# Kernel tuning notes

Hardware: AMD Instinct MI355X
Metric: run time of the kernel (lower is better)

The kernel has to match this reference:

```python
import jax, jax.numpy as jnp
import numpy as np

HIDDEN = 1024
HEADS = 16
HEAD_DIM = HIDDEN // HEADS  # 64


def setup_inputs() -> dict:
    key = jax.random.key(0)
    kx, kqkv, ko = jax.random.split(key, 3)
    x = jax.random.normal(kx, (2, 2048, HIDDEN), dtype=jnp.float32)
    # Xavier-uniform init like the torch module; torch Linear weight is [out, in]
    lim_qkv = float(np.sqrt(6.0 / (HIDDEN + 3 * HIDDEN)))
    qkv_w = jax.random.uniform(kqkv, (3 * HIDDEN, HIDDEN), minval=-lim_qkv, maxval=lim_qkv, dtype=jnp.float32)
    qkv_b = jnp.zeros((3 * HIDDEN,), dtype=jnp.float32)
    lim_o = float(np.sqrt(6.0 / (HIDDEN + HIDDEN)))
    o_w = jax.random.uniform(ko, (HIDDEN, HIDDEN), minval=-lim_o, maxval=lim_o, dtype=jnp.float32)
    o_b = jnp.zeros((HIDDEN,), dtype=jnp.float32)
    return {"x": x, "qkv_w": qkv_w, "qkv_b": qkv_b, "o_w": o_w, "o_b": o_b}


def reference(x, qkv_w, qkv_b, o_w, o_b):
    B, S, D = x.shape
    H, Dh = HEADS, HEAD_DIM
    # qkv projection (torch Linear: x @ W.T + b) -> [B, S, 3*D]
    qkv = jnp.einsum('bsd,ed->bse', x, qkv_w) + qkv_b
    # reshape to [B, H, S, 3*Dh] then split into q, k, v
    qkv = qkv.reshape(B, S, H, 3 * Dh).transpose(0, 2, 1, 3)
    q, k, v = jnp.split(qkv, 3, axis=-1)  # each [B, H, S, Dh]
    # scaled dot-product attention, materializing full [B, H, S, S] scores
    logits = jnp.einsum('bhqd,bhkd->bhqk', q, k) / jnp.sqrt(jnp.asarray(Dh, x.dtype))
    attn = jax.nn.softmax(logits, axis=-1)
    values = jnp.einsum('bhqk,bhkd->bhqd', attn, v)
    # merge heads -> [B, S, D], then output projection
    values = values.transpose(0, 2, 1, 3).reshape(B, S, D)
    return jnp.einsum('bsd,ed->bse', values, o_w) + o_b
```

## Files before the change

kernel.cpp:

```cpp
#include <hip/hip_runtime.h>
#include <hip/hip_bf16.h>

#define BDIM 2
#define SEQ  2048
#define HID  1024
#define NH   16
#define HD   64
#define MROWS (BDIM * SEQ)
#define QKVN  (3 * HID)
#define QBLK 128

typedef __attribute__((ext_vector_type(8))) short s8b;
typedef __attribute__((ext_vector_type(4))) float f4;

__device__ __forceinline__ unsigned f2bf(float f) {
    unsigned u = __builtin_bit_cast(unsigned, f);
    return (u + 0x7FFFu + ((u >> 16) & 1u)) >> 16;
}
__device__ __forceinline__ float bf2f(unsigned h) {
    return __builtin_bit_cast(float, h << 16);
}

__global__ __launch_bounds__(256) void split_hi_lo(
    const float* __restrict__ src, unsigned short* __restrict__ hi,
    unsigned short* __restrict__ lo, int n8)
{
    const int i = blockIdx.x * 256 + threadIdx.x;
    if (i >= n8) return;
    const float4* s = (const float4*)src + 2 * (size_t)i;
    float4 a = s[0], b = s[1];
    const float v[8] = {a.x, a.y, a.z, a.w, b.x, b.y, b.z, b.w};
    unsigned hu[8], lu[8];
#pragma unroll
    for (int j = 0; j < 8; ++j) {
        hu[j] = f2bf(v[j]);
        lu[j] = f2bf(v[j] - bf2f(hu[j]));
    }
    uint4 hv = {hu[0] | (hu[1] << 16), hu[2] | (hu[3] << 16),
                hu[4] | (hu[5] << 16), hu[6] | (hu[7] << 16)};
    uint4 lv = {lu[0] | (lu[1] << 16), lu[2] | (lu[3] << 16),
                lu[4] | (lu[5] << 16), lu[6] | (lu[7] << 16)};
    *((uint4*)hi + i) = hv;
    *((uint4*)lo + i) = lv;
}

template <int OUTBF>
__global__ __launch_bounds__(256)
__attribute__((amdgpu_waves_per_eu(2, 2)))
void gemm_split(
    const unsigned short* __restrict__ Ah, const unsigned short* __restrict__ Al,
    const unsigned short* __restrict__ Wh, const unsigned short* __restrict__ Wl,
    const float* __restrict__ bias, void* __restrict__ Cout, int N, int K)
{
    const int t   = threadIdx.x;
    const int l   = t & 63;
    const int l15 = t & 15;
    const int lg  = (t >> 4) & 3;
    const int w   = t >> 6;
    const int wr  = w >> 1, wc = w & 1;
    const int bm  = blockIdx.y * 128, bn = blockIdx.x * 128;

    __shared__ unsigned short SB[2][4][128 * 32];

    f4 acc[4][4];
#pragma unroll
    for (int i = 0; i < 4; ++i)
#pragma unroll
        for (int j = 0; j < 4; ++j) acc[i][j] = (f4){0.f, 0.f, 0.f, 0.f};

    const unsigned short* plane_src = (w == 0) ? Ah : (w == 1) ? Al
                                    : (w == 2) ? Wh : Wl;
    const int rb0 = (w < 2) ? bm : bn;
    const int gsw = ((l & 3) ^ ((l >> 2) & 3)) * 8;

    auto stage = [&](int buf, int k0) {
        const unsigned short* gp =
            plane_src + (size_t)(rb0 + (l >> 2)) * K + k0 + gsw;
        unsigned short* lb = &SB[buf][w][0];
#pragma unroll
        for (int c = 0; c < 8; ++c)
            __builtin_amdgcn_global_load_lds(
                (const __attribute__((address_space(1))) void*)(gp + (size_t)(c * 16) * K),
                (__attribute__((address_space(3))) void*)(lb + c * 512),
                16, 0, 0);
    };

    const int ksw = ((lg ^ (l15 & 3)) & 3) << 3;

    stage(0, 0);
    __syncthreads();

    int cur = 0;
    const int nsteps = K >> 5;
    for (int step = 0; step < nsteps; ++step) {
        if (step + 1 < nsteps) stage(cur ^ 1, (step + 1) << 5);

        const unsigned short* base = &SB[cur][0][0];
        s8b bh[4], bl[4];
#pragma unroll
        for (int nt = 0; nt < 4; ++nt) {
            const int ro = (wc * 64 + nt * 16 + l15) * 32 + ksw;
            bh[nt] = *(const s8b*)(base + 2 * 4096 + ro);
            bl[nt] = *(const s8b*)(base + 3 * 4096 + ro);
        }
#pragma unroll
        for (int mt = 0; mt < 4; ++mt) {
            const int ro = (wr * 64 + mt * 16 + l15) * 32 + ksw;
            s8b ah = *(const s8b*)(base + ro);
            s8b al = *(const s8b*)(base + 4096 + ro);
#pragma unroll
            for (int nt = 0; nt < 4; ++nt) {
                acc[mt][nt] = __builtin_amdgcn_mfma_f32_16x16x32_bf16(ah, bh[nt], acc[mt][nt], 0, 0, 0);
                acc[mt][nt] = __builtin_amdgcn_mfma_f32_16x16x32_bf16(ah, bl[nt], acc[mt][nt], 0, 0, 0);
                acc[mt][nt] = __builtin_amdgcn_mfma_f32_16x16x32_bf16(al, bh[nt], acc[mt][nt], 0, 0, 0);
            }
        }
        __syncthreads();
        cur ^= 1;
    }

    float bv[4];
#pragma unroll
    for (int nt = 0; nt < 4; ++nt) bv[nt] = bias[bn + wc * 64 + nt * 16 + l15];

#pragma unroll
    for (int mt = 0; mt < 4; ++mt)
#pragma unroll
        for (int i = 0; i < 4; ++i) {
            const int m = bm + wr * 64 + mt * 16 + lg * 4 + i;
#pragma unroll
            for (int nt = 0; nt < 4; ++nt) {
                const int n = bn + wc * 64 + nt * 16 + l15;
                const float v = acc[mt][nt][i] + bv[nt];
                if (OUTBF)
                    ((unsigned short*)Cout)[(size_t)m * N + n] = (unsigned short)f2bf(v);
                else
                    ((float*)Cout)[(size_t)m * N + n] = v;
            }
        }
}

__device__ __forceinline__ int sw_off(int row, int colbyte) {
    return row * 128 + (colbyte ^ ((((row & 7) ^ (row >> 3)) & 7) << 4));
}

__global__ __launch_bounds__(256) void transpose_v(
    const unsigned short* __restrict__ qkv, unsigned short* __restrict__ vt)
{
    const int bh = blockIdx.y;
    const int b  = bh >> 4, h = bh & 15;
    const int s0 = blockIdx.x * 64;
    const int t  = threadIdx.x;

    __shared__ unsigned short T[64 * 64];

#pragma unroll
    for (int rep = 0; rep < 2; ++rep) {
        const int idx = t + rep * 256;
        const int srow = idx >> 3, gg = idx & 7;
        uint4 v = *(const uint4*)(qkv + (size_t)(b * SEQ + s0 + srow) * QKVN
                                  + h * (3 * HD) + 2 * HD + gg * 8);
        *(uint4*)((char*)T + sw_off(srow, gg * 16)) = v;
    }
    __syncthreads();
#pragma unroll
    for (int rep = 0; rep < 2; ++rep) {
        const int idx = t + rep * 256;
        const int drow = idx >> 3, gg = idx & 7;
        unsigned short tmp[8];
#pragma unroll
        for (int j = 0; j < 8; ++j)
            tmp[j] = *(const unsigned short*)((const char*)T + sw_off(gg * 8 + j, drow * 2));
        *(uint4*)(vt + ((size_t)bh * 64 + drow) * SEQ + s0 + gg * 8) = *(const uint4*)tmp;
    }
}

__global__ __launch_bounds__(512) void attn_fwd_mfma(
    const unsigned short* __restrict__ qkv,
    const unsigned short* __restrict__ vt,
    unsigned short* __restrict__ att_hi, unsigned short* __restrict__ att_lo)
{
    const int t   = threadIdx.x;
    const int w   = t >> 6;
    const int l   = t & 63;
    const int l15 = l & 15;
    const int lg  = l >> 4;

    const int bh = blockIdx.y;
    const int b  = bh >> 4;
    const int h  = bh & 15;
    const int q0 = blockIdx.x * QBLK;

    __shared__ unsigned short Ks[64 * 64];
    __shared__ unsigned short Vt[64 * 64];
    __shared__ unsigned short Ps[QBLK * 64];

    const unsigned short* base  = qkv + (size_t)b * SEQ * QKVN + h * (3 * HD);
    const unsigned short* vbase = vt + (size_t)bh * 64 * SEQ;

    s8b qf[2];
    {
        const unsigned short* qrow = base + (size_t)(q0 + w * 16 + l15) * QKVN;
        qf[0] = *(const s8b*)(qrow + lg * 8);
        qf[1] = *(const s8b*)(qrow + 32 + lg * 8);
    }

    float m_run[4], l_run[4];
    f4 oacc[4];
#pragma unroll
    for (int i = 0; i < 4; ++i) {
        m_run[i] = -1e30f;
        l_run[i] = 0.f;
        oacc[i]  = (f4){0.f, 0.f, 0.f, 0.f};
    }

    const int srow = t >> 3;
    const int sgg  = t & 7;

    for (int kt = 0; kt < SEQ; kt += 64) {
        __syncthreads();

        uint4 kg = *(const uint4*)(base + (size_t)(kt + srow) * QKVN + HD + sgg * 8);
        *(uint4*)((char*)Ks + sw_off(srow, sgg * 16)) = kg;
        uint4 vg = *(const uint4*)(vbase + (size_t)srow * SEQ + kt + sgg * 8);
        *(uint4*)((char*)Vt + sw_off(srow, sgg * 16)) = vg;
        __syncthreads();

        f4 sacc[4];
#pragma unroll
        for (int nt = 0; nt < 4; ++nt) sacc[nt] = (f4){0.f, 0.f, 0.f, 0.f};
#pragma unroll
        for (int kc = 0; kc < 2; ++kc) {
            const int colb = kc * 64 + lg * 16;
#pragma unroll
            for (int nt = 0; nt < 4; ++nt) {
                s8b kf = *(const s8b*)((const char*)Ks + sw_off(nt * 16 + l15, colb));
                sacc[nt] = __builtin_amdgcn_mfma_f32_16x16x32_bf16(qf[kc], kf, sacc[nt], 0, 0, 0);
            }
        }
        const float SCL = 0.125f * 1.44269504088896f;
#pragma unroll
        for (int nt = 0; nt < 4; ++nt)
#pragma unroll
            for (int i = 0; i < 4; ++i) sacc[nt][i] *= SCL;

        float mt4[4];
#pragma unroll
        for (int i = 0; i < 4; ++i)
            mt4[i] = fmaxf(fmaxf(sacc[0][i], sacc[1][i]), fmaxf(sacc[2][i], sacc[3][i]));
#pragma unroll
        for (int s = 1; s <= 8; s <<= 1)
#pragma unroll
            for (int i = 0; i < 4; ++i)
                mt4[i] = fmaxf(mt4[i], __shfl_xor(mt4[i], s));

        bool grew = (mt4[0] > m_run[0]) | (mt4[1] > m_run[1]) |
                    (mt4[2] > m_run[2]) | (mt4[3] > m_run[3]);
        if (__any(grew)) {
#pragma unroll
            for (int i = 0; i < 4; ++i) {
                const float mn  = fmaxf(m_run[i], mt4[i]);
                const float cor = exp2f(m_run[i] - mn);
                m_run[i] = mn;
                l_run[i] *= cor;
#pragma unroll
                for (int nt = 0; nt < 4; ++nt) oacc[nt][i] *= cor;
            }
        }

        float rs[4] = {0.f, 0.f, 0.f, 0.f};
        const int rowbase = w * 16 + lg * 4;
#pragma unroll
        for (int nt = 0; nt < 4; ++nt) {
#pragma unroll
            for (int i = 0; i < 4; ++i) {
                const float p = exp2f(sacc[nt][i] - m_run[i]);
                rs[i] += p;
                *(unsigned short*)((char*)Ps + sw_off(rowbase + i, (nt * 16 + l15) * 2)) =
                    (unsigned short)f2bf(p);
            }
        }
#pragma unroll
        for (int s = 1; s <= 8; s <<= 1)
#pragma unroll
            for (int i = 0; i < 4; ++i)
                rs[i] += __shfl_xor(rs[i], s);
#pragma unroll
        for (int i = 0; i < 4; ++i) l_run[i] += rs[i];

#pragma unroll
        for (int kk = 0; kk < 2; ++kk) {
            const int colb = kk * 64 + lg * 16;
            s8b pf = *(const s8b*)((const char*)Ps + sw_off(w * 16 + l15, colb));
#pragma unroll
            for (int nt = 0; nt < 4; ++nt) {
                s8b vf = *(const s8b*)((const char*)Vt + sw_off(nt * 16 + l15, colb));
                oacc[nt] = __builtin_amdgcn_mfma_f32_16x16x32_bf16(pf, vf, oacc[nt], 0, 0, 0);
            }
        }
    }

    float inv[4];
#pragma unroll
    for (int i = 0; i < 4; ++i) inv[i] = 1.f / l_run[i];
#pragma unroll
    for (int i = 0; i < 4; ++i) {
        const size_t rowb = (size_t)(b * SEQ + q0 + w * 16 + lg * 4 + i) * HID + h * HD + l15;
#pragma unroll
        for (int nt = 0; nt < 4; ++nt) {
            const float v = oacc[nt][i] * inv[i];
            const unsigned hu = f2bf(v);
            const unsigned lu = f2bf(v - bf2f(hu));
            att_hi[rowb + nt * 16] = (unsigned short)hu;
            att_lo[rowb + nt * 16] = (unsigned short)lu;
        }
    }
}

extern "C" void kernel_launch(void* const* d_in, const int* in_sizes, int n_in,
                              void* d_out, int out_size, void* d_ws, size_t ws_size,
                              hipStream_t stream) {
    const float* x     = (const float*)d_in[0];
    const float* qkv_w = (const float*)d_in[1];
    const float* qkv_b = (const float*)d_in[2];
    const float* o_w   = (const float*)d_in[3];
    const float* o_b   = (const float*)d_in[4];
    float* out = (float*)d_out;

    char* ws = (char*)d_ws;
    unsigned short* qkv_bf = (unsigned short*)ws;   ws += (size_t)MROWS * QKVN * 2;
    unsigned short* wh     = (unsigned short*)ws;   ws += (size_t)QKVN * HID * 2;
    unsigned short* wl     = (unsigned short*)ws;   ws += (size_t)QKVN * HID * 2;
    unsigned short* owh    = (unsigned short*)ws;   ws += (size_t)HID * HID * 2;
    unsigned short* owl    = (unsigned short*)ws;   ws += (size_t)HID * HID * 2;
    unsigned short* xh     = (unsigned short*)ws;   ws += (size_t)MROWS * HID * 2;
    unsigned short* xl     = (unsigned short*)ws;   ws += (size_t)MROWS * HID * 2;
    unsigned short* vt     = (unsigned short*)ws;
    unsigned short* att_hi = xh;
    unsigned short* att_lo = xl;

    split_hi_lo<<<(MROWS * HID / 8) / 256, 256, 0, stream>>>(x, xh, xl, MROWS * HID / 8);
    split_hi_lo<<<(QKVN * HID / 8) / 256, 256, 0, stream>>>(qkv_w, wh, wl, QKVN * HID / 8);
    split_hi_lo<<<(HID * HID / 8) / 256, 256, 0, stream>>>(o_w, owh, owl, HID * HID / 8);

    gemm_split<1><<<dim3(QKVN / 128, MROWS / 128), 256, 0, stream>>>(
        xh, xl, wh, wl, qkv_b, qkv_bf, QKVN, HID);

    transpose_v<<<dim3(SEQ / 64, BDIM * NH), 256, 0, stream>>>(qkv_bf, vt);

    attn_fwd_mfma<<<dim3(SEQ / QBLK, BDIM * NH), 512, 0, stream>>>(
        qkv_bf, vt, att_hi, att_lo);

    gemm_split<0><<<dim3(HID / 128, MROWS / 128), 256, 0, stream>>>(
        att_hi, att_lo, owh, owl, o_b, out, HID, HID);

    (void)in_sizes; (void)n_in; (void)out_size; (void)ws_size;
}
```

Baseline: 319.1 us.

## Double-buffer K/V tiles in attention kernel with register prefetch and block swizzle

The attention kernel now keeps two LDS buffers for K and V. The next tile is loaded from global memory into registers while the current tile is being computed, and is written to the other buffer at the end of the iteration, so one barrier per iteration replaces two. The softmax scale is folded into an fma inside exp2 instead of a separate multiply pass, and MFMA sections are wrapped in s_setprio. Blocks are remapped so that consecutive block ids cover different heads, and bf16 conversion of P uses the HIP intrinsic. LDS use grows by 16KB and register pressure rises from the held prefetch.

```diff
diff --git a/kernel.cpp b/kernel.cpp
--- a/kernel.cpp
+++ b/kernel.cpp
@@ -19,6 +19,9 @@
 }
 __device__ __forceinline__ float bf2f(unsigned h) {
     return __builtin_bit_cast(float, h << 16);
+}
+__device__ __forceinline__ unsigned short f2bf_s(float f) {
+    return __builtin_bit_cast(unsigned short, __float2bfloat16(f));
 }
 
 __global__ __launch_bounds__(256) void split_hi_lo(
@@ -186,13 +189,15 @@
     const int l15 = l & 15;
     const int lg  = l >> 4;
 
-    const int bh = blockIdx.y;
+    const int id = blockIdx.y * 16 + blockIdx.x;
+    const int bh = (id & 7) * 4 + ((id >> 3) & 3);
+    const int qx = id >> 5;
     const int b  = bh >> 4;
     const int h  = bh & 15;
-    const int q0 = blockIdx.x * QBLK;
-
-    __shared__ unsigned short Ks[64 * 64];
-    __shared__ unsigned short Vt[64 * 64];
+    const int q0 = qx * QBLK;
+
+    __shared__ unsigned short Ks[2][64 * 64];
+    __shared__ unsigned short Vt[2][64 * 64];
     __shared__ unsigned short Ps[QBLK * 64];
 
     const unsigned short* base  = qkv + (size_t)b * SEQ * QKVN + h * (3 * HD);
@@ -216,33 +221,41 @@
 
     const int srow = t >> 3;
     const int sgg  = t & 7;
+    const int kofs = sw_off(srow, sgg * 16);
+
+    {
+        uint4 kg = *(const uint4*)(base + (size_t)srow * QKVN + HD + sgg * 8);
+        uint4 vg = *(const uint4*)(vbase + (size_t)srow * SEQ + sgg * 8);
+        *(uint4*)((char*)&Ks[0][0] + kofs) = kg;
+        *(uint4*)((char*)&Vt[0][0] + kofs) = vg;
+    }
+    __syncthreads();
+
+    const float SCL = 0.125f * 1.44269504088896f;
+    int cur = 0;
 
     for (int kt = 0; kt < SEQ; kt += 64) {
-        __syncthreads();
-
-        uint4 kg = *(const uint4*)(base + (size_t)(kt + srow) * QKVN + HD + sgg * 8);
-        *(uint4*)((char*)Ks + sw_off(srow, sgg * 16)) = kg;
-        uint4 vg = *(const uint4*)(vbase + (size_t)srow * SEQ + kt + sgg * 8);
-        *(uint4*)((char*)Vt + sw_off(srow, sgg * 16)) = vg;
-        __syncthreads();
+        const bool has_next = (kt + 64 < SEQ);
+        uint4 kg, vg;
+        if (has_next) {
+            kg = *(const uint4*)(base + (size_t)(kt + 64 + srow) * QKVN + HD + sgg * 8);
+            vg = *(const uint4*)(vbase + (size_t)srow * SEQ + kt + 64 + sgg * 8);
+        }
 
         f4 sacc[4];
 #pragma unroll
         for (int nt = 0; nt < 4; ++nt) sacc[nt] = (f4){0.f, 0.f, 0.f, 0.f};
+        __builtin_amdgcn_s_setprio(1);
 #pragma unroll
         for (int kc = 0; kc < 2; ++kc) {
             const int colb = kc * 64 + lg * 16;
 #pragma unroll
             for (int nt = 0; nt < 4; ++nt) {
-                s8b kf = *(const s8b*)((const char*)Ks + sw_off(nt * 16 + l15, colb));
+                s8b kf = *(const s8b*)((const char*)&Ks[cur][0] + sw_off(nt * 16 + l15, colb));
                 sacc[nt] = __builtin_amdgcn_mfma_f32_16x16x32_bf16(qf[kc], kf, sacc[nt], 0, 0, 0);
             }
         }
-        const float SCL = 0.125f * 1.44269504088896f;
-#pragma unroll
-        for (int nt = 0; nt < 4; ++nt)
-#pragma unroll
-            for (int i = 0; i < 4; ++i) sacc[nt][i] *= SCL;
+        __builtin_amdgcn_s_setprio(0);
 
         float mt4[4];
 #pragma unroll
@@ -260,7 +273,7 @@
 #pragma unroll
             for (int i = 0; i < 4; ++i) {
                 const float mn  = fmaxf(m_run[i], mt4[i]);
-                const float cor = exp2f(m_run[i] - mn);
+                const float cor = exp2f((m_run[i] - mn) * SCL);
                 m_run[i] = mn;
                 l_run[i] *= cor;
 #pragma unroll
@@ -268,16 +281,19 @@
             }
         }
 
-        float rs[4] = {0.f, 0.f, 0.f, 0.f};
+        float msc[4], rs[4];
+#pragma unroll
+        for (int i = 0; i < 4; ++i) { msc[i] = m_run[i] * SCL; rs[i] = 0.f; }
+
         const int rowbase = w * 16 + lg * 4;
 #pragma unroll
         for (int nt = 0; nt < 4; ++nt) {
 #pragma unroll
             for (int i = 0; i < 4; ++i) {
-                const float p = exp2f(sacc[nt][i] - m_run[i]);
+                const float p = exp2f(fmaf(sacc[nt][i], SCL, -msc[i]));
                 rs[i] += p;
                 *(unsigned short*)((char*)Ps + sw_off(rowbase + i, (nt * 16 + l15) * 2)) =
-                    (unsigned short)f2bf(p);
+                    f2bf_s(p);
             }
         }
 #pragma unroll
@@ -288,16 +304,25 @@
 #pragma unroll
         for (int i = 0; i < 4; ++i) l_run[i] += rs[i];
 
+        __builtin_amdgcn_s_setprio(1);
 #pragma unroll
         for (int kk = 0; kk < 2; ++kk) {
             const int colb = kk * 64 + lg * 16;
             s8b pf = *(const s8b*)((const char*)Ps + sw_off(w * 16 + l15, colb));
 #pragma unroll
             for (int nt = 0; nt < 4; ++nt) {
-                s8b vf = *(const s8b*)((const char*)Vt + sw_off(nt * 16 + l15, colb));
+                s8b vf = *(const s8b*)((const char*)&Vt[cur][0] + sw_off(nt * 16 + l15, colb));
                 oacc[nt] = __builtin_amdgcn_mfma_f32_16x16x32_bf16(pf, vf, oacc[nt], 0, 0, 0);
             }
         }
+        __builtin_amdgcn_s_setprio(0);
+
+        if (has_next) {
+            *(uint4*)((char*)&Ks[cur ^ 1][0] + kofs) = kg;
+            *(uint4*)((char*)&Vt[cur ^ 1][0] + kofs) = vg;
+        }
+        __syncthreads();
+        cur ^= 1;
     }
 
     float inv[4];
```

Measured after the change: 311.0 us. -2.5%, faster.
